# Kernel tuning notes

Measured on AMD Instinct MI355X. Metric: run time of the kernel, lower is better.

Reference implementation:

```python
import jax, jax.numpy as jnp
import numpy as np

EPS = 1e-5  # BatchNorm1d default eps


def setup_inputs() -> dict:
    key = jax.random.key(0)
    k1, k2 = jax.random.split(key)
    B, T, F = 32, 4096, 256
    x = jax.random.normal(k1, (B, T, F), dtype=jnp.float32)
    mask = jax.random.randint(k2, (B, T), 0, 2, dtype=jnp.int32)
    gamma = jnp.ones((F,), dtype=jnp.float32)
    beta = jnp.zeros((F,), dtype=jnp.float32)
    return {"x": x, "mask": mask, "gamma": gamma, "beta": beta}


def reference(x, mask, gamma, beta):
    # Training-mode MaskedNorm: BatchNorm1d statistics over masked (mask>0)
    # positions only; normalized values scattered back, unmasked positions
    # keep the original x (masked_scatter semantics).
    B, T, F = x.shape
    m = (mask > 0).astype(x.dtype)[..., None]          # [B, T, 1]
    count = jnp.sum(m)                                  # scalar, number of selected rows
    mean = jnp.sum(x * m, axis=(0, 1)) / count          # [F]
    var = jnp.sum(((x - mean) ** 2) * m, axis=(0, 1)) / count  # biased var, [F]
    normed = (x - mean) * jax.lax.rsqrt(var + EPS) * gamma + beta
    return jnp.where(m > 0, normed, x)
```

## Files before the change

### kernel.cpp

```cpp
#include <hip/hip_runtime.h>

#define EPS 1e-5f

constexpr int F    = 256;
constexpr int F4   = 64;
constexpr int ROWS = 32 * 4096;
constexpr int NG   = ROWS / 32;

typedef float vfloat4 __attribute__((ext_vector_type(4)));

__global__ void __launch_bounds__(256, 4) reduce_kernel(
    const float4* __restrict__ x4, const int4* __restrict__ mask4,
    float* __restrict__ pS1, float* __restrict__ pS2,
    float* __restrict__ pCnt, int nblk)
{
    const int lane = threadIdx.x & 63;
    const int wv   = threadIdx.x >> 6;

    float4 s1 = {0.f, 0.f, 0.f, 0.f};
    float4 s2 = {0.f, 0.f, 0.f, 0.f};
    float  cnt = 0.f;

    for (int g = blockIdx.x; g < NG; g += nblk) {
        const int row0 = g * 32 + wv * 8;
        const int4 mlo = mask4[(row0 >> 2) + 0];
        const int4 mhi = mask4[(row0 >> 2) + 1];
        const int m[8] = {mlo.x, mlo.y, mlo.z, mlo.w, mhi.x, mhi.y, mhi.z, mhi.w};
        const float4* p = x4 + (size_t)row0 * F4 + lane;

        float4 v[8];
        #pragma unroll
        for (int j = 0; j < 8; ++j)
            if (m[j] > 0) v[j] = p[j * F4];
        #pragma unroll
        for (int j = 0; j < 8; ++j)
            if (m[j] > 0) {
                const float4 w = v[j];
                s1.x += w.x; s1.y += w.y; s1.z += w.z; s1.w += w.w;
                s2.x = fmaf(w.x, w.x, s2.x); s2.y = fmaf(w.y, w.y, s2.y);
                s2.z = fmaf(w.z, w.z, s2.z); s2.w = fmaf(w.w, w.w, s2.w);
                cnt += 1.f;
            }
    }

    __shared__ float4 sh1[256];
    __shared__ float4 sh2[256];
    __shared__ float  shc[4];
    sh1[threadIdx.x] = s1;
    sh2[threadIdx.x] = s2;
    if (lane == 0) shc[wv] = cnt;
    __syncthreads();

    if (wv == 0) {
        float4 a = sh1[lane];
        float4 b = sh2[lane];
        #pragma unroll
        for (int w = 1; w < 4; ++w) {
            const float4 c = sh1[w * 64 + lane];
            const float4 d = sh2[w * 64 + lane];
            a.x += c.x; a.y += c.y; a.z += c.z; a.w += c.w;
            b.x += d.x; b.y += d.y; b.z += d.z; b.w += d.w;
        }
        const int f0  = lane * 4;
        const int blk = blockIdx.x;
        pS1[(size_t)(f0 + 0) * nblk + blk] = a.x;
        pS1[(size_t)(f0 + 1) * nblk + blk] = a.y;
        pS1[(size_t)(f0 + 2) * nblk + blk] = a.z;
        pS1[(size_t)(f0 + 3) * nblk + blk] = a.w;
        pS2[(size_t)(f0 + 0) * nblk + blk] = b.x;
        pS2[(size_t)(f0 + 1) * nblk + blk] = b.y;
        pS2[(size_t)(f0 + 2) * nblk + blk] = b.z;
        pS2[(size_t)(f0 + 3) * nblk + blk] = b.w;
        if (lane == 0)
            pCnt[blk] = shc[0] + shc[1] + shc[2] + shc[3];
    }
}

__global__ void __launch_bounds__(64) finalize_kernel(
    const float* __restrict__ pS1, const float* __restrict__ pS2,
    const float* __restrict__ pCnt,
    const float* __restrict__ gamma, const float* __restrict__ beta,
    float* __restrict__ scale, float* __restrict__ shift, int nblk)
{
    const int f = blockIdx.x;
    const int t = threadIdx.x;

    const float* c1 = pS1 + (size_t)f * nblk;
    const float* c2 = pS2 + (size_t)f * nblk;

    float s1 = 0.f, s2 = 0.f, c = 0.f;
    for (int b = t; b < nblk; b += 64) {
        s1 += c1[b];
        s2 += c2[b];
        c  += pCnt[b];
    }
    #pragma unroll
    for (int off = 32; off > 0; off >>= 1) {
        s1 += __shfl_down(s1, off);
        s2 += __shfl_down(s2, off);
        c  += __shfl_down(c,  off);
    }
    if (t == 0) {
        const float inv_cnt = 1.f / c;
        const float mean = s1 * inv_cnt;
        const float var  = fmaf(-mean, mean, s2 * inv_cnt);
        const float inv  = rsqrtf(var + EPS);
        const float g    = gamma[f] * inv;
        scale[f] = g;
        shift[f] = fmaf(-mean, g, beta[f]);
    }
}

__device__ __forceinline__ vfloat4 sel4(int m, const float4 v,
                                        const float4 sc, const float4 sh)
{
    vfloat4 o;
    o.x = (m > 0) ? fmaf(v.x, sc.x, sh.x) : v.x;
    o.y = (m > 0) ? fmaf(v.y, sc.y, sh.y) : v.y;
    o.z = (m > 0) ? fmaf(v.z, sc.z, sh.z) : v.z;
    o.w = (m > 0) ? fmaf(v.w, sc.w, sh.w) : v.w;
    return o;
}

__global__ void __launch_bounds__(256, 4) norm_kernel(
    const float4* __restrict__ x4, const int4* __restrict__ mask4,
    const float4* __restrict__ scale4, const float4* __restrict__ shift4,
    float4* __restrict__ out4)
{
    const int lane = threadIdx.x & 63;
    const int wv   = threadIdx.x >> 6;
    const float4 sc = scale4[lane];
    const float4 sh = shift4[lane];

    vfloat4* __restrict__ outv = reinterpret_cast<vfloat4*>(out4);

    for (int g = blockIdx.x; g < NG; g += gridDim.x) {
        const int row0 = g * 32 + wv * 8;
        const int4 mlo = mask4[(row0 >> 2) + 0];
        const int4 mhi = mask4[(row0 >> 2) + 1];
        const int m[8] = {mlo.x, mlo.y, mlo.z, mlo.w, mhi.x, mhi.y, mhi.z, mhi.w};
        const size_t base = (size_t)row0 * F4 + lane;

        float4 v[8];
        #pragma unroll
        for (int j = 0; j < 8; ++j) v[j] = x4[base + (size_t)j * F4];
        #pragma unroll
        for (int j = 0; j < 8; ++j)
            __builtin_nontemporal_store(sel4(m[j], v[j], sc, sh),
                                        &outv[base + (size_t)j * F4]);
    }
}

extern "C" void kernel_launch(void* const* d_in, const int* in_sizes, int n_in,
                              void* d_out, int out_size, void* d_ws, size_t ws_size,
                              hipStream_t stream)
{
    const float* x     = (const float*)d_in[0];
    const int*   mask  = (const int*)d_in[1];
    const float* gamma = (const float*)d_in[2];
    const float* beta  = (const float*)d_in[3];
    float* out = (float*)d_out;
    float* ws  = (float*)d_ws;

    int nblk = 1024;
    while (nblk > 4 &&
           ((size_t)nblk * F * 2 + nblk + 512) * sizeof(float) > ws_size)
        nblk >>= 1;

    float* pS1   = ws;
    float* pS2   = pS1 + (size_t)F * nblk;
    float* pCnt  = pS2 + (size_t)F * nblk;
    float* scale = pCnt + nblk;
    float* shift = scale + F;

    reduce_kernel<<<nblk, 256, 0, stream>>>(
        (const float4*)x, (const int4*)mask, pS1, pS2, pCnt, nblk);
    finalize_kernel<<<F, 64, 0, stream>>>(
        pS1, pS2, pCnt, gamma, beta, scale, shift, nblk);
    norm_kernel<<<1024, 256, 0, stream>>>(
        (const float4*)x, (const int4*)mask, (const float4*)scale,
        (const float4*)shift, (float4*)out);
}
```

Baseline: 252.8 us.

## Fuse finalize into reduce kernel via last-block ticket and fix block count

Merges the finalize step into the reduction kernel: each block writes its partial sums contiguously, then takes an atomic ticket, and the last block to finish sums all partials and computes scale and shift. The grid size becomes a compile-time constant, so the row loop has a fixed trip count and can be fully unrolled. This removes one kernel launch and the strided partial-sum writes. In exchange, a memset is added, the final reduction runs serially in a single block over 1024 partials, and the workspace-size fallback is gone.

```diff
diff --git a/kernel.cpp b/kernel.cpp
--- a/kernel.cpp
+++ b/kernel.cpp
@@ -6,22 +6,36 @@
 constexpr int F4   = 64;
 constexpr int ROWS = 32 * 4096;
 constexpr int NG   = ROWS / 32;
+constexpr int NBLK = 1024;
+constexpr int ITER = NG / NBLK;
 
 typedef float vfloat4 __attribute__((ext_vector_type(4)));
 
-__global__ void __launch_bounds__(256, 4) reduce_kernel(
+__global__ void __launch_bounds__(256, 4) reduce_finalize_kernel(
     const float4* __restrict__ x4, const int4* __restrict__ mask4,
+    const float* __restrict__ gamma, const float* __restrict__ beta,
     float* __restrict__ pS1, float* __restrict__ pS2,
-    float* __restrict__ pCnt, int nblk)
+    float* __restrict__ pCnt,
+    float* __restrict__ scale, float* __restrict__ shift,
+    unsigned int* __restrict__ ticket)
 {
     const int lane = threadIdx.x & 63;
     const int wv   = threadIdx.x >> 6;
+    const int bid  = blockIdx.x;
+
+    __shared__ float4 sh1[256];
+    __shared__ float4 sh2[256];
+    __shared__ float  shc[4];
+    __shared__ int    isLast;
+    __shared__ float  cntAll;
 
     float4 s1 = {0.f, 0.f, 0.f, 0.f};
     float4 s2 = {0.f, 0.f, 0.f, 0.f};
     float  cnt = 0.f;
 
-    for (int g = blockIdx.x; g < NG; g += nblk) {
+    #pragma unroll
+    for (int i = 0; i < ITER; ++i) {
+        const int g    = bid + i * NBLK;
         const int row0 = g * 32 + wv * 8;
         const int4 mlo = mask4[(row0 >> 2) + 0];
         const int4 mhi = mask4[(row0 >> 2) + 1];
@@ -43,9 +57,6 @@
             }
     }
 
-    __shared__ float4 sh1[256];
-    __shared__ float4 sh2[256];
-    __shared__ float  shc[4];
     sh1[threadIdx.x] = s1;
     sh2[threadIdx.x] = s2;
     if (lane == 0) shc[wv] = cnt;
@@ -61,54 +72,46 @@
             a.x += c.x; a.y += c.y; a.z += c.z; a.w += c.w;
             b.x += d.x; b.y += d.y; b.z += d.z; b.w += d.w;
         }
-        const int f0  = lane * 4;
-        const int blk = blockIdx.x;
-        pS1[(size_t)(f0 + 0) * nblk + blk] = a.x;
-        pS1[(size_t)(f0 + 1) * nblk + blk] = a.y;
-        pS1[(size_t)(f0 + 2) * nblk + blk] = a.z;
-        pS1[(size_t)(f0 + 3) * nblk + blk] = a.w;
-        pS2[(size_t)(f0 + 0) * nblk + blk] = b.x;
-        pS2[(size_t)(f0 + 1) * nblk + blk] = b.y;
-        pS2[(size_t)(f0 + 2) * nblk + blk] = b.z;
-        pS2[(size_t)(f0 + 3) * nblk + blk] = b.w;
+        reinterpret_cast<float4*>(pS1)[bid * F4 + lane] = a;
+        reinterpret_cast<float4*>(pS2)[bid * F4 + lane] = b;
         if (lane == 0)
-            pCnt[blk] = shc[0] + shc[1] + shc[2] + shc[3];
+            pCnt[bid] = shc[0] + shc[1] + shc[2] + shc[3];
     }
-}
+    __syncthreads();
 
-__global__ void __launch_bounds__(64) finalize_kernel(
-    const float* __restrict__ pS1, const float* __restrict__ pS2,
-    const float* __restrict__ pCnt,
-    const float* __restrict__ gamma, const float* __restrict__ beta,
-    float* __restrict__ scale, float* __restrict__ shift, int nblk)
-{
-    const int f = blockIdx.x;
+    if (threadIdx.x == 0) {
+        __threadfence();
+        const unsigned int old = atomicAdd(ticket, 1u);
+        isLast = (old == (unsigned int)(gridDim.x - 1)) ? 1 : 0;
+    }
+    __syncthreads();
+    if (!isLast) return;
+
+    __threadfence();
     const int t = threadIdx.x;
 
-    const float* c1 = pS1 + (size_t)f * nblk;
-    const float* c2 = pS2 + (size_t)f * nblk;
+    float a = 0.f, b = 0.f;
+    #pragma unroll 8
+    for (int bk = 0; bk < NBLK; ++bk) {
+        a += pS1[bk * F + t];
+        b += pS2[bk * F + t];
+    }
+    float c = pCnt[t] + pCnt[t + 256] + pCnt[t + 512] + pCnt[t + 768];
+    #pragma unroll
+    for (int off = 32; off > 0; off >>= 1)
+        c += __shfl_down(c, off);
+    if (lane == 0) shc[wv] = c;
+    __syncthreads();
+    if (t == 0) cntAll = shc[0] + shc[1] + shc[2] + shc[3];
+    __syncthreads();
 
-    float s1 = 0.f, s2 = 0.f, c = 0.f;
-    for (int b = t; b < nblk; b += 64) {
-        s1 += c1[b];
-        s2 += c2[b];
-        c  += pCnt[b];
-    }
-    #pragma unroll
-    for (int off = 32; off > 0; off >>= 1) {
-        s1 += __shfl_down(s1, off);
-        s2 += __shfl_down(s2, off);
-        c  += __shfl_down(c,  off);
-    }
-    if (t == 0) {
-        const float inv_cnt = 1.f / c;
-        const float mean = s1 * inv_cnt;
-        const float var  = fmaf(-mean, mean, s2 * inv_cnt);
-        const float inv  = rsqrtf(var + EPS);
-        const float g    = gamma[f] * inv;
-        scale[f] = g;
-        shift[f] = fmaf(-mean, g, beta[f]);
-    }
+    const float inv_cnt = 1.f / cntAll;
+    const float mean = a * inv_cnt;
+    const float var  = fmaf(-mean, mean, b * inv_cnt);
+    const float inv  = rsqrtf(var + EPS);
+    const float g    = gamma[t] * inv;
+    scale[t] = g;
+    shift[t] = fmaf(-mean, g, beta[t]);
 }
 
 __device__ __forceinline__ vfloat4 sel4(int m, const float4 v,
@@ -162,22 +165,19 @@
     float* out = (float*)d_out;
     float* ws  = (float*)d_ws;
 
-    int nblk = 1024;
-    while (nblk > 4 &&
-           ((size_t)nblk * F * 2 + nblk + 512) * sizeof(float) > ws_size)
-        nblk >>= 1;
+    float* pS1   = ws;
+    float* pS2   = pS1 + (size_t)NBLK * F;
+    float* pCnt  = pS2 + (size_t)NBLK * F;
+    float* scale = pCnt + NBLK;
+    float* shift = scale + F;
+    unsigned int* ticket = (unsigned int*)(shift + F);
 
-    float* pS1   = ws;
-    float* pS2   = pS1 + (size_t)F * nblk;
-    float* pCnt  = pS2 + (size_t)F * nblk;
-    float* scale = pCnt + nblk;
-    float* shift = scale + F;
+    hipMemsetAsync(ticket, 0, sizeof(unsigned int), stream);
 
-    reduce_kernel<<<nblk, 256, 0, stream>>>(
-        (const float4*)x, (const int4*)mask, pS1, pS2, pCnt, nblk);
-    finalize_kernel<<<F, 64, 0, stream>>>(
-        pS1, pS2, pCnt, gamma, beta, scale, shift, nblk);
-    norm_kernel<<<1024, 256, 0, stream>>>(
-        (const float4*)x, (const int4*)mask, (const float4*)scale,
-        (const float4*)shift, (float4*)out);
+    reduce_finalize_kernel<<<NBLK, 256, 0, stream>>>(
+        (const float4*)x, (const int4*)mask, gamma, beta,
+        pS1, pS2, pCnt, scale, shift, ticket);
+    norm_kernel<<<NBLK, 256, 0, stream>>>(
+        (const float4*)x, (const int4*)mask,
+        (const float4*)scale, (const float4*)shift, (float4*)out);
 }
```

Measured after the change: 321.5 us. 1.27x slower.
